# Kernel optimization log

Measured on AMD Instinct MI355X. Metric: run time of the kernel, lower is better.

The kernel has to match this reference:

```python
import jax, jax.numpy as jnp
import numpy as np

THR = 0.2
BORDER_RM = 2
TEMP = 0.1


def _border_valid(n, b):
    idx = jnp.arange(n)
    return (idx >= b) & (idx < n - b)


def setup_inputs() -> dict:
    key = jax.random.key(0)
    k0, k1 = jax.random.split(key)
    N, L, S, C = 4, 3600, 3600, 256
    return {
        "feat_c0": jax.random.normal(k0, (N, L, C), dtype=jnp.float32),
        "feat_c1": jax.random.normal(k1, (N, S, C), dtype=jnp.float32),
        "h0c": 60, "w0c": 60, "h1c": 60, "w1c": 60,
    }


def reference(feat_c0, feat_c1, h0c, w0c, h1c, w1c):
    N, L, C = feat_c0.shape
    S = feat_c1.shape[1]
    inv_sqrt_c = 1.0 / (C ** 0.5)
    f0 = feat_c0 * inv_sqrt_c
    f1 = feat_c1 * inv_sqrt_c
    # [N, L, S] similarity, temperature 0.1
    sim = jnp.einsum('nlc,nsc->nls', f0, f1) / TEMP
    conf = jax.nn.softmax(sim, axis=1) * jax.nn.softmax(sim, axis=2)

    # threshold mask + border removal (applied in [b,h0,w0,h1,w1] layout,
    # expressed here as separable 1D validity masks -- same result, no 5D copy churn)
    v0h = _border_valid(h0c, BORDER_RM)  # [h0c]
    v0w = _border_valid(w0c, BORDER_RM)
    v1h = _border_valid(h1c, BORDER_RM)
    v1w = _border_valid(w1c, BORDER_RM)
    valid_l = (v0h[:, None] & v0w[None, :]).reshape(L)   # [L]
    valid_s = (v1h[:, None] & v1w[None, :]).reshape(S)   # [S]
    mask = (conf > THR) & valid_l[None, :, None] & valid_s[None, None, :]

    # mutual nearest (dual argmax equality)
    mask = mask & (conf == conf.max(axis=2, keepdims=True)) & (conf == conf.max(axis=1, keepdims=True))

    # fixed-shape match extraction: per (b, i) row, is there a match and where
    mask_v = jnp.any(mask, axis=2)                       # [N, L] bool
    all_j_ids = jnp.argmax(mask, axis=2)                 # [N, L] int
    mconf = jnp.take_along_axis(conf, all_j_ids[:, :, None], axis=2)[:, :, 0]
    mconf = jnp.where(mask_v, mconf, 0.0)                # [N, L]
    return conf, mask_v, all_j_ids, mconf
```

## Files before the change

### kernel.cpp

```cpp
#include <hip/hip_runtime.h>
#include <stdint.h>


typedef _Float16 f16;
typedef _Float16 f16x8 __attribute__((ext_vector_type(8)));
typedef float f32x4 __attribute__((ext_vector_type(4)));

#define N_B 4
#define L_DIM 3600
#define S_DIM 3600
#define C_DIM 256

#define P1_THREADS 192
#define P1_BM 144
#define P1_BN 48
#define P1_ITERS 5
#define P1_CHUNK 240
#define P1_NCH 15
#define P1_NRT 25

#define C_EXP1 (0.0390625f * 1.4426950408889634f)
#define C_EXP2 (0.0781250f * 1.4426950408889634f)

__global__ void cast_kernel(const float* __restrict__ a, const float* __restrict__ b,
                            f16* __restrict__ ah, f16* __restrict__ bh, int total8) {
  int i = blockIdx.x * blockDim.x + threadIdx.x;
  if (i >= total8) return;
  const float4* a4 = (const float4*)a;
  const float4* b4 = (const float4*)b;
  float4 x = a4[2 * (size_t)i], y = a4[2 * (size_t)i + 1];
  f16x8 o = {(f16)x.x, (f16)x.y, (f16)x.z, (f16)x.w,
             (f16)y.x, (f16)y.y, (f16)y.z, (f16)y.w};
  *(f16x8*)(ah + 8 * (size_t)i) = o;
  x = b4[2 * (size_t)i]; y = b4[2 * (size_t)i + 1];
  f16x8 o2 = {(f16)x.x, (f16)x.y, (f16)x.z, (f16)x.w,
              (f16)y.x, (f16)y.y, (f16)y.z, (f16)y.w};
  *(f16x8*)(bh + 8 * (size_t)i) = o2;
}

__global__ __launch_bounds__(P1_THREADS, 3) void gemm_stats_kernel(
    const f16* __restrict__ X, const f16* __restrict__ Y,
    float* __restrict__ den_r, float* __restrict__ den_c) {
  __shared__ float colsum_w[3][P1_CHUNK];
  const int rt = blockIdx.x, ch = blockIdx.y, n = blockIdx.z;
  const int tid = threadIdx.x;
  const int wave = tid >> 6, lane = tid & 63;
  const int q = lane >> 4, r = lane & 15;
  const int l0 = rt * P1_BM;
  const int s0 = ch * P1_CHUNK;

  f16x8 a[3][8];
#pragma unroll
  for (int grp = 0; grp < 3; ++grp) {
    const f16* xrow = X + ((size_t)n * L_DIM + l0 + wave * 48 + grp * 16 + r) * C_DIM;
#pragma unroll
    for (int k = 0; k < 8; ++k) a[grp][k] = *(const f16x8*)(xrow + k * 32 + q * 8);
  }

  float sum_e[3][4];
#pragma unroll
  for (int grp = 0; grp < 3; ++grp)
#pragma unroll
    for (int g = 0; g < 4; ++g) sum_e[grp][g] = 0.f;

  const f16* ybase = Y + ((size_t)n * S_DIM + s0) * C_DIM;

  for (int it = 0; it < P1_ITERS; ++it) {
    f32x4 acc[3][3];
#pragma unroll
    for (int grp = 0; grp < 3; ++grp)
#pragma unroll
      for (int nt = 0; nt < 3; ++nt) acc[grp][nt] = (f32x4){0.f, 0.f, 0.f, 0.f};

#pragma unroll
    for (int k = 0; k < 8; ++k) {
#pragma unroll
      for (int nt = 0; nt < 3; ++nt) {
        f16x8 b = *(const f16x8*)(ybase +
            (size_t)(it * P1_BN + nt * 16 + r) * C_DIM + k * 32 + q * 8);
#pragma unroll
        for (int grp = 0; grp < 3; ++grp)
          acc[grp][nt] = __builtin_amdgcn_mfma_f32_16x16x32_f16(a[grp][k], b, acc[grp][nt], 0, 0, 0);
      }
    }

#pragma unroll
    for (int nt = 0; nt < 3; ++nt) {
      float csum = 0.f;
#pragma unroll
      for (int grp = 0; grp < 3; ++grp) {
#pragma unroll
        for (int g = 0; g < 4; ++g) {
          float e = exp2f(acc[grp][nt][g] * C_EXP1);
          sum_e[grp][g] += e;
          csum += e;
        }
      }
      csum += __shfl_xor(csum, 16, 64);
      csum += __shfl_xor(csum, 32, 64);
      if (q == 0) colsum_w[wave][it * P1_BN + nt * 16 + r] = csum;
    }
  }

#pragma unroll
  for (int m = 1; m < 16; m <<= 1)
#pragma unroll
    for (int grp = 0; grp < 3; ++grp)
#pragma unroll
      for (int g = 0; g < 4; ++g) sum_e[grp][g] += __shfl_xor(sum_e[grp][g], m, 64);
  if (r == 0) {
#pragma unroll
    for (int grp = 0; grp < 3; ++grp)
#pragma unroll
      for (int g = 0; g < 4; ++g)
        atomicAdd(&den_r[n * L_DIM + l0 + wave * 48 + grp * 16 + q * 4 + g], sum_e[grp][g]);
  }

  __syncthreads();
  for (int i = tid; i < P1_CHUNK; i += P1_THREADS)
    atomicAdd(&den_c[n * S_DIM + s0 + i],
              colsum_w[0][i] + colsum_w[1][i] + colsum_w[2][i]);
}

__global__ void invert_kernel(float* __restrict__ a, float* __restrict__ b) {
  int i = blockIdx.x * blockDim.x + threadIdx.x;
  if (i >= N_B * L_DIM) return;
  a[i] = 1.0f / a[i];
  b[i] = 1.0f / b[i];
}

__global__ __launch_bounds__(P1_THREADS, 3) void gemm_conf_kernel(
    const f16* __restrict__ X, const f16* __restrict__ Y,
    const float* __restrict__ invdr, const float* __restrict__ invdc,
    float* __restrict__ conf_out,
    unsigned long long* __restrict__ rowarg,
    unsigned int* __restrict__ colmax_bits) {
  __shared__ __attribute__((aligned(16))) float colmax_w[3][P1_CHUNK];
  const int rt = blockIdx.x, ch = blockIdx.y, n = blockIdx.z;
  const int tid = threadIdx.x;
  const int wave = tid >> 6, lane = tid & 63;
  const int q = lane >> 4, r = lane & 15;
  const int l0 = rt * P1_BM;
  const int s0 = ch * P1_CHUNK;

  f16x8 a[3][8];
#pragma unroll
  for (int grp = 0; grp < 3; ++grp) {
    const f16* xrow = X + ((size_t)n * L_DIM + l0 + wave * 48 + grp * 16 + r) * C_DIM;
#pragma unroll
    for (int k = 0; k < 8; ++k) a[grp][k] = *(const f16x8*)(xrow + k * 32 + q * 8);
  }

  float idr[3];
#pragma unroll
  for (int grp = 0; grp < 3; ++grp)
    idr[grp] = invdr[n * L_DIM + l0 + wave * 48 + grp * 16 + r];

  float mx[3];
  int mj[3];
#pragma unroll
  for (int i = 0; i < 3; ++i) { mx[i] = 0.f; mj[i] = 0; }

  float* cbase = conf_out + ((size_t)n * L_DIM + l0 + wave * 48) * S_DIM;
  const float* idcb = invdc + n * S_DIM + s0;
  const f16* ybase = Y + ((size_t)n * S_DIM + s0) * C_DIM;

  for (int it = 0; it < P1_ITERS; ++it) {
    f32x4 acc[3][3];
#pragma unroll
    for (int grp = 0; grp < 3; ++grp)
#pragma unroll
      for (int nt = 0; nt < 3; ++nt) acc[grp][nt] = (f32x4){0.f, 0.f, 0.f, 0.f};

#pragma unroll
    for (int k = 0; k < 8; ++k) {
#pragma unroll
      for (int nt = 0; nt < 3; ++nt) {
        f16x8 b = *(const f16x8*)(ybase +
            (size_t)(it * P1_BN + nt * 16 + r) * C_DIM + k * 32 + q * 8);
#pragma unroll
        for (int grp = 0; grp < 3; ++grp)
          acc[grp][nt] = __builtin_amdgcn_mfma_f32_16x16x32_f16(b, a[grp][k], acc[grp][nt], 0, 0, 0);
      }
    }

#pragma unroll
    for (int nt = 0; nt < 3; ++nt) {
      const int lc = it * P1_BN + nt * 16 + q * 4;
      const int sc = s0 + lc;
      const float4 idc4 = *(const float4*)(idcb + lc);
      f32x4 cmx = {0.f, 0.f, 0.f, 0.f};
#pragma unroll
      for (int grp = 0; grp < 3; ++grp) {
        f32x4 w;
        w.x = exp2f(acc[grp][nt][0] * C_EXP2) * (idc4.x * idr[grp]);
        w.y = exp2f(acc[grp][nt][1] * C_EXP2) * (idc4.y * idr[grp]);
        w.z = exp2f(acc[grp][nt][2] * C_EXP2) * (idc4.z * idr[grp]);
        w.w = exp2f(acc[grp][nt][3] * C_EXP2) * (idc4.w * idr[grp]);
        __builtin_nontemporal_store(w,
            (f32x4*)(cbase + (size_t)(grp * 16 + r) * S_DIM + sc));
        if (w.x > mx[grp]) { mx[grp] = w.x; mj[grp] = sc; }
        if (w.y > mx[grp]) { mx[grp] = w.y; mj[grp] = sc + 1; }
        if (w.z > mx[grp]) { mx[grp] = w.z; mj[grp] = sc + 2; }
        if (w.w > mx[grp]) { mx[grp] = w.w; mj[grp] = sc + 3; }
        cmx.x = fmaxf(cmx.x, w.x);
        cmx.y = fmaxf(cmx.y, w.y);
        cmx.z = fmaxf(cmx.z, w.z);
        cmx.w = fmaxf(cmx.w, w.w);
      }
#pragma unroll
      for (int m = 1; m < 16; m <<= 1) {
        cmx.x = fmaxf(cmx.x, __shfl_xor(cmx.x, m, 64));
        cmx.y = fmaxf(cmx.y, __shfl_xor(cmx.y, m, 64));
        cmx.z = fmaxf(cmx.z, __shfl_xor(cmx.z, m, 64));
        cmx.w = fmaxf(cmx.w, __shfl_xor(cmx.w, m, 64));
      }
      if (r == 0) *(f32x4*)&colmax_w[wave][lc] = cmx;
    }
  }

#pragma unroll
  for (int m = 16; m < 64; m <<= 1) {
#pragma unroll
    for (int grp = 0; grp < 3; ++grp) {
      float ov = __shfl_xor(mx[grp], m, 64);
      int oj = __shfl_xor(mj[grp], m, 64);
      if (ov > mx[grp] || (ov == mx[grp] && oj < mj[grp])) { mx[grp] = ov; mj[grp] = oj; }
    }
  }
  if (q == 0) {
#pragma unroll
    for (int grp = 0; grp < 3; ++grp) {
      unsigned long long key =
          ((unsigned long long)__float_as_uint(mx[grp]) << 32) |
          (unsigned int)(~(unsigned int)mj[grp]);
      atomicMax(&rowarg[n * L_DIM + l0 + wave * 48 + grp * 16 + r], key);
    }
  }

  __syncthreads();
  for (int i = tid; i < P1_CHUNK; i += P1_THREADS) {
    float m3 = fmaxf(fmaxf(colmax_w[0][i], colmax_w[1][i]), colmax_w[2][i]);
    atomicMax(&colmax_bits[n * S_DIM + s0 + i], __float_as_uint(m3));
  }
}

__global__ void finalize_kernel(const unsigned long long* __restrict__ rowarg,
                                const float* __restrict__ colmax,
                                const int* __restrict__ h0c, const int* __restrict__ w0c,
                                const int* __restrict__ h1c, const int* __restrict__ w1c,
                                float* __restrict__ out_maskv, float* __restrict__ out_jids,
                                float* __restrict__ out_mconf) {
  int i = blockIdx.x * blockDim.x + threadIdx.x;
  if (i >= N_B * L_DIM) return;
  int n = i / L_DIM, l = i - n * L_DIM;
  unsigned long long key = rowarg[i];
  float rm = __uint_as_float((unsigned int)(key >> 32));
  int j = (int)(~(unsigned int)key);
  int W0 = *w0c, H0 = *h0c, W1 = *w1c, H1 = *h1c;
  int li = l / W0, lj = l - li * W0;
  bool vl = (li >= 2) && (li < H0 - 2) && (lj >= 2) && (lj < W0 - 2);
  int si = j / W1, sj = j - si * W1;
  bool vs = (si >= 2) && (si < H1 - 2) && (sj >= 2) && (sj < W1 - 2);
  float cm = colmax[n * S_DIM + j];
  bool mv = (rm > 0.2f) && vl && vs &&
            (__float_as_uint(rm) == __float_as_uint(cm));
  out_maskv[i] = mv ? 1.0f : 0.0f;
  out_jids[i]  = mv ? (float)j : 0.0f;
  out_mconf[i] = mv ? rm : 0.0f;
}

extern "C" void kernel_launch(void* const* d_in, const int* in_sizes, int n_in,
                              void* d_out, int out_size, void* d_ws, size_t ws_size,
                              hipStream_t stream) {
  const float* f0 = (const float*)d_in[0];
  const float* f1 = (const float*)d_in[1];
  const int* h0c = (const int*)d_in[2];
  const int* w0c = (const int*)d_in[3];
  const int* h1c = (const int*)d_in[4];
  const int* w1c = (const int*)d_in[5];

  char* ws = (char*)d_ws;
  size_t o = 0;
  f16* f0h = (f16*)(ws + o);               o += (size_t)N_B * L_DIM * C_DIM * 2;
  f16* f1h = (f16*)(ws + o);               o += (size_t)N_B * S_DIM * C_DIM * 2;
  float* den_r = (float*)(ws + o);         o += (size_t)N_B * L_DIM * 4;
  float* den_c = (float*)(ws + o);         o += (size_t)N_B * S_DIM * 4;
  unsigned long long* rowarg = (unsigned long long*)(ws + o); o += (size_t)N_B * L_DIM * 8;
  float* colmax = (float*)(ws + o);        o += (size_t)N_B * S_DIM * 4;
  size_t zero_bytes = (size_t)N_B * (L_DIM * 4 + S_DIM * 4 + L_DIM * 8 + S_DIM * 4);

  float* conf = (float*)d_out;
  float* out_maskv = conf + (size_t)N_B * L_DIM * S_DIM;
  float* out_jids = out_maskv + N_B * L_DIM;
  float* out_mconf = out_jids + N_B * L_DIM;

  hipMemsetAsync(den_r, 0, zero_bytes, stream);

  int total8 = N_B * L_DIM * C_DIM / 8;
  cast_kernel<<<dim3((total8 + 255) / 256), 256, 0, stream>>>(f0, f1, f0h, f1h, total8);

  dim3 g1(P1_NRT, P1_NCH, N_B);
  gemm_stats_kernel<<<g1, P1_THREADS, 0, stream>>>(f0h, f1h, den_r, den_c);
  invert_kernel<<<(N_B * L_DIM + 255) / 256, 256, 0, stream>>>(den_r, den_c);
  gemm_conf_kernel<<<g1, P1_THREADS, 0, stream>>>(
      f0h, f1h, den_r, den_c, conf, rowarg, (unsigned int*)colmax);
  finalize_kernel<<<(N_B * L_DIM + 255) / 256, 256, 0, stream>>>(
      rowarg, colmax, h0c, w0c, h1c, w1c, out_maskv, out_jids, out_mconf);
}
```

Before: 456.2 us.

## Stream X fragments per k-step, prefetch Y, shrink S chunk, raise occupancy

Both GEMM kernels stop holding the full 3x8 A-fragment array in registers and instead reload the X fragments from global/L2 at every k-step. They also software-prefetch the next k-slice of Y. The S chunk per block drops from 240 to 144 columns (25 chunks instead of 15), and launch bounds ask for 4 blocks per CU instead of 3. The aim is lower register pressure and higher occupancy to hide latency, at the cost of re-reading X on every iteration and more blocks doing atomics.

```diff
diff --git a/kernel.cpp b/kernel.cpp
--- a/kernel.cpp
+++ b/kernel.cpp
@@ -14,9 +14,9 @@
 #define P1_THREADS 192
 #define P1_BM 144
 #define P1_BN 48
-#define P1_ITERS 5
-#define P1_CHUNK 240
-#define P1_NCH 15
+#define P1_ITERS 3
+#define P1_CHUNK 144
+#define P1_NCH 25
 #define P1_NRT 25
 
 #define C_EXP1 (0.0390625f * 1.4426950408889634f)
@@ -38,7 +38,7 @@
   *(f16x8*)(bh + 8 * (size_t)i) = o2;
 }
 
-__global__ __launch_bounds__(P1_THREADS, 3) void gemm_stats_kernel(
+__global__ __launch_bounds__(P1_THREADS, 4) void gemm_stats_kernel(
     const f16* __restrict__ X, const f16* __restrict__ Y,
     float* __restrict__ den_r, float* __restrict__ den_c) {
   __shared__ float colsum_w[3][P1_CHUNK];
@@ -49,13 +49,9 @@
   const int l0 = rt * P1_BM;
   const int s0 = ch * P1_CHUNK;
 
-  f16x8 a[3][8];
-#pragma unroll
-  for (int grp = 0; grp < 3; ++grp) {
-    const f16* xrow = X + ((size_t)n * L_DIM + l0 + wave * 48 + grp * 16 + r) * C_DIM;
-#pragma unroll
-    for (int k = 0; k < 8; ++k) a[grp][k] = *(const f16x8*)(xrow + k * 32 + q * 8);
-  }
+  const f16* xrow0 = X + ((size_t)n * L_DIM + l0 + wave * 48 + 0 * 16 + r) * C_DIM + q * 8;
+  const f16* xrow1 = xrow0 + 16 * C_DIM;
+  const f16* xrow2 = xrow1 + 16 * C_DIM;
 
   float sum_e[3][4];
 #pragma unroll
@@ -63,7 +59,7 @@
 #pragma unroll
     for (int g = 0; g < 4; ++g) sum_e[grp][g] = 0.f;
 
-  const f16* ybase = Y + ((size_t)n * S_DIM + s0) * C_DIM;
+  const f16* ybase = Y + ((size_t)n * S_DIM + s0) * C_DIM + q * 8;
 
   for (int it = 0; it < P1_ITERS; ++it) {
     f32x4 acc[3][3];
@@ -72,16 +68,29 @@
 #pragma unroll
       for (int nt = 0; nt < 3; ++nt) acc[grp][nt] = (f32x4){0.f, 0.f, 0.f, 0.f};
 
+    f16x8 yb[3], ybn[3];
+#pragma unroll
+    for (int nt = 0; nt < 3; ++nt)
+      yb[nt] = *(const f16x8*)(ybase + (size_t)(it * P1_BN + nt * 16 + r) * C_DIM);
+
 #pragma unroll
     for (int k = 0; k < 8; ++k) {
-#pragma unroll
-      for (int nt = 0; nt < 3; ++nt) {
-        f16x8 b = *(const f16x8*)(ybase +
-            (size_t)(it * P1_BN + nt * 16 + r) * C_DIM + k * 32 + q * 8);
+      f16x8 xa[3];
+      xa[0] = *(const f16x8*)(xrow0 + k * 32);
+      xa[1] = *(const f16x8*)(xrow1 + k * 32);
+      xa[2] = *(const f16x8*)(xrow2 + k * 32);
+      if (k < 7) {
+#pragma unroll
+        for (int nt = 0; nt < 3; ++nt)
+          ybn[nt] = *(const f16x8*)(ybase + (size_t)(it * P1_BN + nt * 16 + r) * C_DIM + (k + 1) * 32);
+      }
+#pragma unroll
+      for (int nt = 0; nt < 3; ++nt)
 #pragma unroll
         for (int grp = 0; grp < 3; ++grp)
-          acc[grp][nt] = __builtin_amdgcn_mfma_f32_16x16x32_f16(a[grp][k], b, acc[grp][nt], 0, 0, 0);
-      }
+          acc[grp][nt] = __builtin_amdgcn_mfma_f32_16x16x32_f16(xa[grp], yb[nt], acc[grp][nt], 0, 0, 0);
+#pragma unroll
+      for (int nt = 0; nt < 3; ++nt) yb[nt] = ybn[nt];
     }
 
 #pragma unroll
@@ -129,7 +138,7 @@
   b[i] = 1.0f / b[i];
 }
 
-__global__ __launch_bounds__(P1_THREADS, 3) void gemm_conf_kernel(
+__global__ __launch_bounds__(P1_THREADS, 4) void gemm_conf_kernel(
     const f16* __restrict__ X, const f16* __restrict__ Y,
     const float* __restrict__ invdr, const float* __restrict__ invdc,
     float* __restrict__ conf_out,
@@ -143,13 +152,9 @@
   const int l0 = rt * P1_BM;
   const int s0 = ch * P1_CHUNK;
 
-  f16x8 a[3][8];
-#pragma unroll
-  for (int grp = 0; grp < 3; ++grp) {
-    const f16* xrow = X + ((size_t)n * L_DIM + l0 + wave * 48 + grp * 16 + r) * C_DIM;
-#pragma unroll
-    for (int k = 0; k < 8; ++k) a[grp][k] = *(const f16x8*)(xrow + k * 32 + q * 8);
-  }
+  const f16* xrow0 = X + ((size_t)n * L_DIM + l0 + wave * 48 + 0 * 16 + r) * C_DIM + q * 8;
+  const f16* xrow1 = xrow0 + 16 * C_DIM;
+  const f16* xrow2 = xrow1 + 16 * C_DIM;
 
   float idr[3];
 #pragma unroll
@@ -163,7 +168,7 @@
 
   float* cbase = conf_out + ((size_t)n * L_DIM + l0 + wave * 48) * S_DIM;
   const float* idcb = invdc + n * S_DIM + s0;
-  const f16* ybase = Y + ((size_t)n * S_DIM + s0) * C_DIM;
+  const f16* ybase = Y + ((size_t)n * S_DIM + s0) * C_DIM + q * 8;
 
   for (int it = 0; it < P1_ITERS; ++it) {
     f32x4 acc[3][3];
@@ -172,16 +177,29 @@
 #pragma unroll
       for (int nt = 0; nt < 3; ++nt) acc[grp][nt] = (f32x4){0.f, 0.f, 0.f, 0.f};
 
+    f16x8 yb[3], ybn[3];
+#pragma unroll
+    for (int nt = 0; nt < 3; ++nt)
+      yb[nt] = *(const f16x8*)(ybase + (size_t)(it * P1_BN + nt * 16 + r) * C_DIM);
+
 #pragma unroll
     for (int k = 0; k < 8; ++k) {
-#pragma unroll
-      for (int nt = 0; nt < 3; ++nt) {
-        f16x8 b = *(const f16x8*)(ybase +
-            (size_t)(it * P1_BN + nt * 16 + r) * C_DIM + k * 32 + q * 8);
+      f16x8 xa[3];
+      xa[0] = *(const f16x8*)(xrow0 + k * 32);
+      xa[1] = *(const f16x8*)(xrow1 + k * 32);
+      xa[2] = *(const f16x8*)(xrow2 + k * 32);
+      if (k < 7) {
+#pragma unroll
+        for (int nt = 0; nt < 3; ++nt)
+          ybn[nt] = *(const f16x8*)(ybase + (size_t)(it * P1_BN + nt * 16 + r) * C_DIM + (k + 1) * 32);
+      }
+#pragma unroll
+      for (int nt = 0; nt < 3; ++nt)
 #pragma unroll
         for (int grp = 0; grp < 3; ++grp)
-          acc[grp][nt] = __builtin_amdgcn_mfma_f32_16x16x32_f16(b, a[grp][k], acc[grp][nt], 0, 0, 0);
-      }
+          acc[grp][nt] = __builtin_amdgcn_mfma_f32_16x16x32_f16(yb[nt], xa[grp], acc[grp][nt], 0, 0, 0);
+#pragma unroll
+      for (int nt = 0; nt < 3; ++nt) yb[nt] = ybn[nt];
     }
 
 #pragma unroll
```

Measured after the change: 531.5 us. 1.17x slower.
